# Kernel tuning notes

Hardware: AMD Instinct MI355X
Metric: run time of the kernel (lower is better)

## Reference

```python
import jax, jax.numpy as jnp
import numpy as np

WIN_LEN = 400
WIN_INC = 100
FFT_LEN = 512
EPSILON = float(np.finfo(np.float32).eps)


def _make_kernel():
    # periodic (fftbins=True) hamming window, matching scipy.signal.get_window
    n = np.arange(WIN_LEN)
    window = 0.54 - 0.46 * np.cos(2.0 * np.pi * n / WIN_LEN)
    # direct-DFT basis: rfft of identity, truncated to win_len taps
    fourier_basis = np.fft.rfft(np.eye(FFT_LEN))[:WIN_LEN]          # [win_len, fft_len//2+1]
    kernel = np.concatenate([fourier_basis.real, fourier_basis.imag], axis=1).T  # [2*(fft//2+1), win_len]
    kernel = kernel * window                                        # window applied per tap
    return kernel[:, None, :].astype(np.float32)                    # [514, 1, 400] (OIH)


def setup_inputs() -> dict:
    key = jax.random.key(0)
    inputs = jax.random.normal(key, (16, 160000), dtype=jnp.float32)  # [B, L] waveform
    weight = jnp.asarray(_make_kernel())                              # fixed DFT buffer
    return {"inputs": inputs, "weight": weight}


def reference(inputs, weight):
    pad = WIN_LEN - WIN_INC  # 300
    x = inputs[:, None, :]                                   # [B, 1, L]
    x = jnp.pad(x, ((0, 0), (0, 0), (pad, pad)))             # symmetric pad, as in F.pad
    out = jax.lax.conv_general_dilated(
        x, weight,
        window_strides=(WIN_INC,),
        padding='VALID',
        dimension_numbers=('NCH', 'OIH', 'NCH'),
    )                                                        # [B, 514, T]
    r, i = jnp.split(out, 2, axis=1)                         # real / imag halves [B, 257, T]
    mags = jnp.sqrt(jnp.clip(r * r + i * i, EPSILON))
    phase = jnp.arctan2(i + EPSILON, r + EPSILON)
    return mags, phase
```

## Files before the change

### kernel.cpp

```cpp
#include <hip/hip_runtime.h>
#include <math.h>


#define BATCH 16
#define NSAMP 160000
#define NF 257
#define NT 1603
#define KLEN 400
#define INC 100
#define PADL 300
#define EPSF 1.1920928955078125e-7f
#define TAU 1e-2f

#define FPB 16
#define ZSTR 258
#define XSPAN ((FPB - 1) * INC + KLEN)
#define NTB ((NT + FPB - 1) / FPB)

__global__ __launch_bounds__(256, 3)
void stft_fft(const float* __restrict__ x, const float* __restrict__ w,
              float* __restrict__ out) {
  __shared__ float2 Z[FPB * ZSTR];
  __shared__ float2 tw[256];
  __shared__ float y256[FPB];
  __shared__ __align__(16) float xs[XSPAN];
  __shared__ __align__(16) float win[KLEN];

  const int tid = threadIdx.x;
  const int t0 = blockIdx.x * FPB;
  const int b = blockIdx.y;
  const int tl = tid & 15;
  const int th = tid >> 4;

  const long xb = (long)b * NSAMP;
  const int base = t0 * INC - PADL;
  for (int r = 0; r < 2; ++r) {
    int i4 = r * 256 + tid;
    if (4 * i4 < XSPAN) {
      int g = base + 4 * i4;
      float4 v;
      if (g >= 0 && g + 3 < NSAMP) {
        v = *(const float4*)(x + xb + g);
      } else {
        v.x = (g + 0 >= 0 && g + 0 < NSAMP) ? x[xb + g + 0] : 0.f;
        v.y = (g + 1 >= 0 && g + 1 < NSAMP) ? x[xb + g + 1] : 0.f;
        v.z = (g + 2 >= 0 && g + 2 < NSAMP) ? x[xb + g + 2] : 0.f;
        v.w = (g + 3 >= 0 && g + 3 < NSAMP) ? x[xb + g + 3] : 0.f;
      }
      *(float4*)&xs[4 * i4] = v;
    }
  }
  if (tid < KLEN / 4) {
    *(float4*)&win[4 * tid] = *(const float4*)(w + 4 * tid);
  }
  {
    double a = (double)tid * (6.283185307179586476925286766559 / 512.0);
    tw[tid] = make_float2((float)cos(a), (float)(-sin(a)));
  }
  __syncthreads();

  for (int r = 0; r < 16; ++r) {
    int m = r * 16 + th;
    float2 zv = make_float2(0.f, 0.f);
    if (m < 200) {
      float2 xv = *(const float2*)&xs[tl * INC + 2 * m];
      float2 wv = *(const float2*)&win[2 * m];
      zv = make_float2(xv.x * wv.x, xv.y * wv.y);
    }
    int p = __brev((unsigned)m) >> 24;
    Z[tl * ZSTR + p] = zv;
  }

  for (int s = 0; s < 8; ++s) {
    __syncthreads();
    const int half = 1 << s;
    for (int r = 0; r < 8; ++r) {
      int j = r * 16 + th;
      int q = j & (half - 1);
      int i0 = ((j >> s) << (s + 1)) | q;
      float2* Zt = Z + tl * ZSTR;
      float2 a = Zt[i0];
      float2 bb = Zt[i0 + half];
      float2 wv = tw[q << (8 - s)];
      float2 bt = make_float2(bb.x * wv.x - bb.y * wv.y,
                              bb.x * wv.y + bb.y * wv.x);
      Zt[i0] = make_float2(a.x + bt.x, a.y + bt.y);
      Zt[i0 + half] = make_float2(a.x - bt.x, a.y - bt.y);
    }
  }
  __syncthreads();

  for (int r = 0; r < 9; ++r) {
    int tau = r * 256 + tid;
    if (tau < FPB * 129) {
      int t = tau & 15;
      int p = tau >> 4;
      float2* Zt = Z + t * ZSTR;
      float2 z0 = Zt[p];
      float2 z1 = Zt[(256 - p) & 255];
      float2 ze = make_float2(0.5f * (z0.x + z1.x), 0.5f * (z0.y - z1.y));
      float2 zo = make_float2(0.5f * (z0.y + z1.y), 0.5f * (z1.x - z0.x));
      float2 T = tw[p];
      float2 tz = make_float2(zo.x * T.x - zo.y * T.y,
                              zo.x * T.y + zo.y * T.x);
      Zt[p] = make_float2(ze.x + tz.x, ze.y + tz.y);
      float2 yb = make_float2(ze.x - tz.x, tz.y - ze.y);
      if (p == 0) y256[t] = yb.x;
      else Zt[256 - p] = yb;
    }
  }
  __syncthreads();

  const long plane = (long)BATCH * NF * NT;
  const long pb = (long)b * NF * NT;
  for (int r = 0; r < 17; ++r) {
    int tau = r * 256 + tid;
    if (tau < NF * FPB) {
      int t = tau & 15;
      int ff = tau >> 4;
      int tt = t0 + t;
      if (tt < NT) {
        float rr, ii;
        if (ff < 256) {
          float2 v = Z[t * ZSTR + ff];
          rr = v.x; ii = v.y;
        } else {
          rr = y256[t]; ii = 0.f;
        }
        float ie = ii + EPSF, re = rr + EPSF;
        if (fabsf(ie) < TAU && re < TAU) {
          const float* wr = w + (long)ff * KLEN;
          const float* wi = w + (long)(257 + ff) * KLEN;
          const float* xf = &xs[t * INC];
          float r2 = 0.f, i2 = 0.f;
          for (int k = 0; k < KLEN; ++k) {
            float xv = xf[k];
            r2 = fmaf(wr[k], xv, r2);
            i2 = fmaf(wi[k], xv, i2);
          }
          rr = r2; ii = i2;
        }
        long o = pb + (long)ff * NT + tt;
        out[o] = sqrtf(fmaxf(rr * rr + ii * ii, EPSF));
        out[o + plane] = atan2f(ii + EPSF, rr + EPSF);
      }
    }
  }
}

extern "C" void kernel_launch(void* const* d_in, const int* in_sizes, int n_in,
                              void* d_out, int out_size, void* d_ws, size_t ws_size,
                              hipStream_t stream) {
  const float* x = (const float*)d_in[0];
  const float* w = (const float*)d_in[1];
  float* out = (float*)d_out;

  dim3 grid(NTB, BATCH);
  stft_fft<<<grid, dim3(256), 0, stream>>>(x, w, out);
}
```

Baseline: 176.4 us.

## Replace shared-memory radix-2 FFT with register/shuffle radix-4 wavefront FFT

Each wavefront now computes a frame's 256-point complex FFT in registers, using an initial radix-4 stage and then cross-lane shuffles. This replaces the shared-memory butterflies and their eight block barriers. Frames per block drop to 8, magnitude and phase are staged in shared memory before coalesced stores, and atan2f is swapped for a polynomial approximation. Block indices are remapped to give XCD-local contiguity. The fast atan2 and the added zero-skip in the fallback path risk small accuracy differences.

```diff
diff --git a/kernel.cpp b/kernel.cpp
--- a/kernel.cpp
+++ b/kernel.cpp
@@ -8,141 +8,204 @@
 #define NT 1603
 #define KLEN 400
 #define INC 100
-#define PADL 300
 #define EPSF 1.1920928955078125e-7f
 #define TAU 1e-2f
 
-#define FPB 16
-#define ZSTR 258
+#define FPB 8
 #define XSPAN ((FPB - 1) * INC + KLEN)
 #define NTB ((NT + FPB - 1) / FPB)
-
-__global__ __launch_bounds__(256, 3)
-void stft_fft(const float* __restrict__ x, const float* __restrict__ w,
-              float* __restrict__ out) {
-  __shared__ float2 Z[FPB * ZSTR];
-  __shared__ float2 tw[256];
-  __shared__ float y256[FPB];
+#define MPLD 257
+
+__device__ __forceinline__ float2 cmul(float2 a, float2 b) {
+  return make_float2(a.x * b.x - a.y * b.y, a.x * b.y + a.y * b.x);
+}
+__device__ __forceinline__ float2 sx(float2 v, int m) {
+  return make_float2(__shfl_xor(v.x, m), __shfl_xor(v.y, m));
+}
+
+__device__ __forceinline__ float fast_atan2(float y, float x) {
+  float ax = fabsf(x), ay = fabsf(y);
+  float mx = fmaxf(ax, ay), mn = fminf(ax, ay);
+  float t = mn * __builtin_amdgcn_rcpf(fmaxf(mx, 1e-37f));
+  float s = t * t;
+  float p = fmaf(s, -0.01172120f, 0.05265332f);
+  p = fmaf(s, p, -0.11643287f);
+  p = fmaf(s, p, 0.19354346f);
+  p = fmaf(s, p, -0.33262347f);
+  p = fmaf(s, p, 0.99997726f);
+  float r = t * p;
+  if (ay > ax) r = 1.57079632679489662f - r;
+  if (x < 0.f) r = 3.14159265358979324f - r;
+  return (y < 0.f) ? -r : r;
+}
+
+__device__ __forceinline__ void emitMP(float rr, float ii, int p, int col,
+                                       const float* xf,
+                                       const float* __restrict__ w,
+                                       float* mrow, float* prow) {
+  float ie = ii + EPSF, re = rr + EPSF;
+  if (fabsf(ie) < TAU && re < TAU && !(rr == 0.f && ii == 0.f)) {
+    const float* wr = w + (long)p * KLEN;
+    const float* wi = w + (long)(257 + p) * KLEN;
+    float r2 = 0.f, i2 = 0.f;
+    for (int k = 0; k < KLEN; ++k) {
+      float xv = xf[k];
+      r2 = fmaf(wr[k], xv, r2);
+      i2 = fmaf(wi[k], xv, i2);
+    }
+    rr = r2; ii = i2;
+  }
+  mrow[col] = sqrtf(fmaxf(rr * rr + ii * ii, EPSF));
+  prow[col] = fast_atan2(ii + EPSF, rr + EPSF);
+}
+
+__device__ __forceinline__ void emitY(float2 z0, float2 z1, float2 T,
+                                      int p, int col, const float* xf,
+                                      const float* __restrict__ w,
+                                      float* mrow, float* prow) {
+  float2 ze = make_float2(0.5f * (z0.x + z1.x), 0.5f * (z0.y - z1.y));
+  float2 zo = make_float2(0.5f * (z0.y + z1.y), 0.5f * (z1.x - z0.x));
+  float2 tz = cmul(zo, T);
+  emitMP(ze.x + tz.x, ze.y + tz.y, p, col, xf, w, mrow, prow);
+}
+
+#define LSTG(VV, HH, MM, TWW) { float2 o_ = sx(VV, MM);                     \
+  float2 su_ = make_float2(VV.x + o_.x, VV.y + o_.y);                       \
+  float2 df_ = make_float2(o_.x - VV.x, o_.y - VV.y);                       \
+  VV = HH ? cmul(df_, TWW) : su_; }
+#define LSTGN(VV, HH, MM) { float2 o_ = sx(VV, MM);                         \
+  float2 su_ = make_float2(VV.x + o_.x, VV.y + o_.y);                       \
+  float2 df_ = make_float2(o_.x - VV.x, o_.y - VV.y);                       \
+  VV = HH ? df_ : su_; }
+
+__global__ __launch_bounds__(256, 4)
+void stft_fft7(const float* __restrict__ x, const float* __restrict__ w,
+               float* __restrict__ out) {
+  __shared__ float magb[FPB * MPLD];
+  __shared__ float phb[FPB * MPLD];
+  __shared__ float2 tw256[256];
   __shared__ __align__(16) float xs[XSPAN];
   __shared__ __align__(16) float win[KLEN];
 
   const int tid = threadIdx.x;
-  const int t0 = blockIdx.x * FPB;
+  const int l = tid & 63;
+  const int wv = tid >> 6;
   const int b = blockIdx.y;
-  const int tl = tid & 15;
-  const int th = tid >> 4;
+
+  const int orig = blockIdx.x;
+  const int xcd = orig & 7;
+  const int tb = ((xcd == 0) ? 0 : (26 + (xcd - 1) * 25)) + (orig >> 3);
+  const int t0 = tb * FPB;
 
   const long xb = (long)b * NSAMP;
-  const int base = t0 * INC - PADL;
-  for (int r = 0; r < 2; ++r) {
-    int i4 = r * 256 + tid;
-    if (4 * i4 < XSPAN) {
-      int g = base + 4 * i4;
-      float4 v;
-      if (g >= 0 && g + 3 < NSAMP) {
-        v = *(const float4*)(x + xb + g);
-      } else {
-        v.x = (g + 0 >= 0 && g + 0 < NSAMP) ? x[xb + g + 0] : 0.f;
-        v.y = (g + 1 >= 0 && g + 1 < NSAMP) ? x[xb + g + 1] : 0.f;
-        v.z = (g + 2 >= 0 && g + 2 < NSAMP) ? x[xb + g + 2] : 0.f;
-        v.w = (g + 3 >= 0 && g + 3 < NSAMP) ? x[xb + g + 3] : 0.f;
-      }
-      *(float4*)&xs[4 * i4] = v;
-    }
+  const int base = t0 * INC - 300;
+  for (int i4 = tid; i4 < XSPAN / 4; i4 += 256) {
+    int g = base + 4 * i4;
+    float4 v;
+    if (g >= 0 && g + 3 < NSAMP) {
+      v = *(const float4*)(x + xb + g);
+    } else {
+      v.x = (g + 0 >= 0 && g + 0 < NSAMP) ? x[xb + g + 0] : 0.f;
+      v.y = (g + 1 >= 0 && g + 1 < NSAMP) ? x[xb + g + 1] : 0.f;
+      v.z = (g + 2 >= 0 && g + 2 < NSAMP) ? x[xb + g + 2] : 0.f;
+      v.w = (g + 3 >= 0 && g + 3 < NSAMP) ? x[xb + g + 3] : 0.f;
+    }
+    *(float4*)&xs[4 * i4] = v;
   }
   if (tid < KLEN / 4) {
     *(float4*)&win[4 * tid] = *(const float4*)(w + 4 * tid);
   }
   {
-    double a = (double)tid * (6.283185307179586476925286766559 / 512.0);
-    tw[tid] = make_float2((float)cos(a), (float)(-sin(a)));
+    double a = (double)tid * (6.283185307179586476925286766559 / 256.0);
+    tw256[tid] = make_float2((float)cos(a), (float)(-sin(a)));
   }
   __syncthreads();
 
-  for (int r = 0; r < 16; ++r) {
-    int m = r * 16 + th;
-    float2 zv = make_float2(0.f, 0.f);
-    if (m < 200) {
-      float2 xv = *(const float2*)&xs[tl * INC + 2 * m];
-      float2 wv = *(const float2*)&win[2 * m];
-      zv = make_float2(xv.x * wv.x, xv.y * wv.y);
-    }
-    int p = __brev((unsigned)m) >> 24;
-    Z[tl * ZSTR + p] = zv;
-  }
-
-  for (int s = 0; s < 8; ++s) {
-    __syncthreads();
-    const int half = 1 << s;
-    for (int r = 0; r < 8; ++r) {
-      int j = r * 16 + th;
-      int q = j & (half - 1);
-      int i0 = ((j >> s) << (s + 1)) | q;
-      float2* Zt = Z + tl * ZSTR;
-      float2 a = Zt[i0];
-      float2 bb = Zt[i0 + half];
-      float2 wv = tw[q << (8 - s)];
-      float2 bt = make_float2(bb.x * wv.x - bb.y * wv.y,
-                              bb.x * wv.y + bb.y * wv.x);
-      Zt[i0] = make_float2(a.x + bt.x, a.y + bt.y);
-      Zt[i0 + half] = make_float2(a.x - bt.x, a.y - bt.y);
+  const int K2 = __brev((unsigned)l) >> 26;
+  const float2 TW0 = tw256[(l & 31) * 4];
+  const float2 TW1 = tw256[(l & 15) * 8];
+  const float2 TW2 = tw256[(l & 7) * 16];
+  const float2 TW3 = tw256[(l & 3) * 32];
+  const float2 TW4 = tw256[(l & 1) * 64];
+  const float2 T1 = tw256[l];
+  const float2 T2 = tw256[2 * l];
+  const float2 T3 = tw256[3 * l];
+  const float2 TB = tw256[2 * K2];
+  const float2 TY0 = TB;
+  const float2 TY1 = cmul(TB, make_float2(0.9999247018391445f, -0.012271538285719925f));
+  const float2 TY2 = cmul(TB, make_float2(0.9996988186962042f, -0.024541228522912288f));
+  const float2 TY3 = cmul(TB, make_float2(0.9993223845883495f, -0.036807222941358832f));
+  const int m0 = __brev((unsigned)((64 - K2) & 63)) >> 26;
+  const bool h32 = l & 32, h16 = l & 16, h8 = l & 8;
+  const bool h4 = l & 4, h2 = l & 2, h1 = l & 1;
+
+  const long plane = (long)BATCH * NF * NT;
+  const long pb = (long)b * NF * NT;
+
+  #pragma unroll 1
+  for (int it = 0; it < 2; ++it) {
+    const int fi = wv * 2 + it;
+    const float* xf = xs + fi * INC;
+
+    float2 z0, z1, z2, z3;
+    { int n = 2 * l;       float2 xv = *(const float2*)&xf[n], wv2 = *(const float2*)&win[n];
+      z0 = make_float2(xv.x * wv2.x, xv.y * wv2.y); }
+    { int n = 2 * l + 128; float2 xv = *(const float2*)&xf[n], wv2 = *(const float2*)&win[n];
+      z1 = make_float2(xv.x * wv2.x, xv.y * wv2.y); }
+    { int n = 2 * l + 256; float2 xv = *(const float2*)&xf[n], wv2 = *(const float2*)&win[n];
+      z2 = make_float2(xv.x * wv2.x, xv.y * wv2.y); }
+    if (l < 8) {
+      int n = 2 * l + 384; float2 xv = *(const float2*)&xf[n], wv2 = *(const float2*)&win[n];
+      z3 = make_float2(xv.x * wv2.x, xv.y * wv2.y);
+    } else z3 = make_float2(0.f, 0.f);
+
+    float2 s02 = make_float2(z0.x + z2.x, z0.y + z2.y);
+    float2 d02 = make_float2(z0.x - z2.x, z0.y - z2.y);
+    float2 s13 = make_float2(z1.x + z3.x, z1.y + z3.y);
+    float2 d13 = make_float2(z1.x - z3.x, z1.y - z3.y);
+    float2 V0 = make_float2(s02.x + s13.x, s02.y + s13.y);
+    float2 V2 = cmul(make_float2(s02.x - s13.x, s02.y - s13.y), T2);
+    float2 V1 = cmul(make_float2(d02.x + d13.y, d02.y - d13.x), T1);
+    float2 V3 = cmul(make_float2(d02.x - d13.y, d02.y + d13.x), T3);
+
+    LSTG(V0, h32, 32, TW0) LSTG(V1, h32, 32, TW0)
+    LSTG(V2, h32, 32, TW0) LSTG(V3, h32, 32, TW0)
+    LSTG(V0, h16, 16, TW1) LSTG(V1, h16, 16, TW1)
+    LSTG(V2, h16, 16, TW1) LSTG(V3, h16, 16, TW1)
+    LSTG(V0, h8,  8,  TW2) LSTG(V1, h8,  8,  TW2)
+    LSTG(V2, h8,  8,  TW2) LSTG(V3, h8,  8,  TW2)
+    LSTG(V0, h4,  4,  TW3) LSTG(V1, h4,  4,  TW3)
+    LSTG(V2, h4,  4,  TW3) LSTG(V3, h4,  4,  TW3)
+    LSTG(V0, h2,  2,  TW4) LSTG(V1, h2,  2,  TW4)
+    LSTG(V2, h2,  2,  TW4) LSTG(V3, h2,  2,  TW4)
+    LSTGN(V0, h1, 1) LSTGN(V1, h1, 1) LSTGN(V2, h1, 1) LSTGN(V3, h1, 1)
+
+    float2 P1 = sx(V1, 63), P2 = sx(V2, 63), P3 = sx(V3, 63);
+    float2 P0 = make_float2(__shfl(V0.x, m0), __shfl(V0.y, m0));
+
+    float* mrow = magb + fi * MPLD;
+    float* prow = phb + fi * MPLD;
+    emitY(V0, P0, TY0, 4 * K2 + 0, K2,       xf, w, mrow, prow);
+    emitY(V1, P3, TY1, 4 * K2 + 1, K2 + 64,  xf, w, mrow, prow);
+    emitY(V2, P2, TY2, 4 * K2 + 2, K2 + 128, xf, w, mrow, prow);
+    emitY(V3, P1, TY3, 4 * K2 + 3, K2 + 192, xf, w, mrow, prow);
+    if (l == 0) {
+      emitMP(V0.x - V0.y, 0.f, 256, 256, xf, w, mrow, prow);
     }
   }
   __syncthreads();
 
   for (int r = 0; r < 9; ++r) {
     int tau = r * 256 + tid;
-    if (tau < FPB * 129) {
-      int t = tau & 15;
-      int p = tau >> 4;
-      float2* Zt = Z + t * ZSTR;
-      float2 z0 = Zt[p];
-      float2 z1 = Zt[(256 - p) & 255];
-      float2 ze = make_float2(0.5f * (z0.x + z1.x), 0.5f * (z0.y - z1.y));
-      float2 zo = make_float2(0.5f * (z0.y + z1.y), 0.5f * (z1.x - z0.x));
-      float2 T = tw[p];
-      float2 tz = make_float2(zo.x * T.x - zo.y * T.y,
-                              zo.x * T.y + zo.y * T.x);
-      Zt[p] = make_float2(ze.x + tz.x, ze.y + tz.y);
-      float2 yb = make_float2(ze.x - tz.x, tz.y - ze.y);
-      if (p == 0) y256[t] = yb.x;
-      else Zt[256 - p] = yb;
-    }
-  }
-  __syncthreads();
-
-  const long plane = (long)BATCH * NF * NT;
-  const long pb = (long)b * NF * NT;
-  for (int r = 0; r < 17; ++r) {
-    int tau = r * 256 + tid;
-    if (tau < NF * FPB) {
-      int t = tau & 15;
-      int ff = tau >> 4;
-      int tt = t0 + t;
+    if (tau < FPB * NF) {
+      int t8 = tau & 7;
+      int p = tau >> 3;
+      int tt = t0 + t8;
       if (tt < NT) {
-        float rr, ii;
-        if (ff < 256) {
-          float2 v = Z[t * ZSTR + ff];
-          rr = v.x; ii = v.y;
-        } else {
-          rr = y256[t]; ii = 0.f;
-        }
-        float ie = ii + EPSF, re = rr + EPSF;
-        if (fabsf(ie) < TAU && re < TAU) {
-          const float* wr = w + (long)ff * KLEN;
-          const float* wi = w + (long)(257 + ff) * KLEN;
-          const float* xf = &xs[t * INC];
-          float r2 = 0.f, i2 = 0.f;
-          for (int k = 0; k < KLEN; ++k) {
-            float xv = xf[k];
-            r2 = fmaf(wr[k], xv, r2);
-            i2 = fmaf(wi[k], xv, i2);
-          }
-          rr = r2; ii = i2;
-        }
-        long o = pb + (long)ff * NT + tt;
-        out[o] = sqrtf(fmaxf(rr * rr + ii * ii, EPSF));
-        out[o + plane] = atan2f(ii + EPSF, rr + EPSF);
+        int col = (p == 256) ? 256 : ((p >> 2) | ((p & 3) << 6));
+        long o = pb + (long)p * NT + tt;
+        out[o] = magb[t8 * MPLD + col];
+        out[o + plane] = phb[t8 * MPLD + col];
       }
     }
   }
@@ -156,5 +219,5 @@
   float* out = (float*)d_out;
 
   dim3 grid(NTB, BATCH);
-  stft_fft<<<grid, dim3(256), 0, stream>>>(x, w, out);
-}
+  stft_fft7<<<grid, dim3(256), 0, stream>>>(x, w, out);
+}
```

After: 232.5 us. +31.8%, slower.
